# Kernel optimization log

Measured on AMD Instinct MI355X. Metric: run time of the kernel, lower is better.

Reference implementation:

```python
import jax, jax.numpy as jnp
import numpy as np

N = 100000   # nodes
E = 3200000  # edges
CIN = 6
H = 256
G = 16       # graphs in batch
EPS = 1e-5


def setup_inputs() -> dict:
    key = jax.random.key(0)
    ks = jax.random.split(key, 16)
    inp = {
        'pos': jax.random.normal(ks[0], (N, 3), dtype=jnp.float32),
        'norm': jax.random.normal(ks[1], (N, 3), dtype=jnp.float32),
        'edge_index': jax.random.randint(ks[2], (2, E), 0, N, dtype=jnp.int64),
        'batch': jnp.sort(jax.random.randint(ks[3], (N,), 0, G, dtype=jnp.int64)),
        'bn0_g': jnp.ones((CIN,), jnp.float32), 'bn0_b': jnp.zeros((CIN,), jnp.float32),
    }
    dims = [(CIN, H), (H, H), (H, H), (H, H)]
    for i, (ci, co) in enumerate(dims, start=1):
        inp[f'W{i}'] = jax.random.normal(ks[3 + i], (ci, co), jnp.float32) * 0.05
        inp[f'b{i}'] = jnp.zeros((co,), jnp.float32)
        inp[f'bn{i}_g'] = jnp.ones((co,), jnp.float32)
        inp[f'bn{i}_b'] = jnp.zeros((co,), jnp.float32)
    return inp


def _bn(x, g, b):
    # BatchNorm1d, training mode: biased batch stats over node dim
    m = jnp.mean(x, axis=0)
    v = jnp.var(x, axis=0)
    return (x - m) * jax.lax.rsqrt(v + EPS) * g + b


def _gcn(x, W, bias, row, col, en, sl):
    # GCNConv: linear -> symmetric-normalized aggregation (with self loops) -> +bias
    xw = x @ W                                             # [N, C_out]
    agg = jax.ops.segment_sum(en[:, None] * xw[row], col, num_segments=N)
    return agg + sl[:, None] * xw + bias


def reference(pos, norm, edge_index, batch,
              bn0_g, bn0_b,
              W1, b1, bn1_g, bn1_b,
              W2, b2, bn2_g, bn2_b,
              W3, b3, bn3_g, bn3_b,
              W4, b4, bn4_g, bn4_b):
    row, col = edge_index[0], edge_index[1]
    # gcn_norm with self loops: deg includes +1 self loop weight
    deg = jax.ops.segment_sum(jnp.ones((E,), jnp.float32), col, num_segments=N) + 1.0
    dinv = jax.lax.rsqrt(deg)
    en = dinv[row] * dinv[col]   # edge norm
    sl = dinv * dinv             # self-loop norm

    x = jnp.concatenate([pos, norm], axis=1)   # [N, 6]
    x = _bn(x, bn0_g, bn0_b)
    for (W, b, g, be) in [(W1, b1, bn1_g, bn1_b), (W2, b2, bn2_g, bn2_b),
                          (W3, b3, bn3_g, bn3_b), (W4, b4, bn4_g, bn4_b)]:
        x = _bn(jax.nn.relu(_gcn(x, W, b, row, col, en, sl)), g, be)

    # global mean pool over graph ids
    sums = jax.ops.segment_sum(x, batch, num_segments=G)
    cnt = jax.ops.segment_sum(jnp.ones((N,), jnp.float32), batch, num_segments=G)
    return sums / jnp.maximum(cnt, 1.0)[:, None]
```

## Files before the change

### kernel.cpp

```cpp
#include <hip/hip_runtime.h>
#include <hip/hip_bf16.h>
#include <cstdint>

#define N_NODES 100000
#define NPAD    100032
#define N_EDGES 3200000
#define HID 256
#define NG 16
#define BN_EPS 1e-5f
#define B0 120
#define NB 391
#define SLABS 128
#define FPART 25000
#define LDSROW 264
#define AGB 2048
#define NGRP (N_NODES / 4)

typedef unsigned short u16;
using bf16x8 = __attribute__((ext_vector_type(8))) short;
using f32x4  = __attribute__((ext_vector_type(4))) float;

__device__ __forceinline__ float bf2f(u16 b) {
    return __uint_as_float(((unsigned)b) << 16);
}
__device__ __forceinline__ u16 f2bf(float f) {
    unsigned u = __float_as_uint(f);
    unsigned r = (u + 0x7FFFu + ((u >> 16) & 1u)) >> 16;
    return (u16)r;
}
__device__ __forceinline__ float4 ld_bf16x4(const u16* p) {
    ushort4 u = *reinterpret_cast<const ushort4*>(p);
    float4 f;
    f.x = bf2f(u.x); f.y = bf2f(u.y); f.z = bf2f(u.z); f.w = bf2f(u.w);
    return f;
}

__global__ void k_count(const int* __restrict__ coli, int* __restrict__ cnt) {
    int i = blockIdx.x * blockDim.x + threadIdx.x;
    int st = gridDim.x * blockDim.x;
    for (; i < N_EDGES; i += st) atomicAdd(&cnt[coli[i]], 1);
}

__global__ __launch_bounds__(256) void k_scanA(const int* __restrict__ cnt,
                                               int* __restrict__ bsum) {
    const int t = threadIdx.x;
    const int i = blockIdx.x * 256 + t;
    int v = (i < N_NODES) ? cnt[i] : 0;
    for (int o = 32; o > 0; o >>= 1) v += __shfl_down(v, o);
    __shared__ int ws[4];
    if ((t & 63) == 0) ws[t >> 6] = v;
    __syncthreads();
    if (t == 0) bsum[blockIdx.x] = ws[0] + ws[1] + ws[2] + ws[3];
}

__global__ __launch_bounds__(512) void k_scanB(const int* __restrict__ bsum,
                                               int* __restrict__ boff,
                                               int* __restrict__ ptrN) {
    const int t = threadIdx.x;
    const int ln = t & 63, wv = t >> 6;
    int v = (t < NB) ? bsum[t] : 0;
    int sc = v;
    for (int o = 1; o < 64; o <<= 1) { int u = __shfl_up(sc, o); if (ln >= o) sc += u; }
    __shared__ int ws[8], wx[9];
    if (ln == 63) ws[wv] = sc;
    __syncthreads();
    if (t == 0) { int a = 0; for (int k = 0; k < 8; ++k) { wx[k] = a; a += ws[k]; } wx[8] = a; }
    __syncthreads();
    int excl = wx[wv] + sc - v;
    if (t < NB) boff[t] = excl;
    if (t == 0) ptrN[0] = wx[8];
}

__global__ __launch_bounds__(256) void k_scanC(const int* __restrict__ cnt,
                                               const int* __restrict__ boff,
                                               int* __restrict__ ptr,
                                               int* __restrict__ ptr2,
                                               float* __restrict__ dinv) {
    const int t = threadIdx.x;
    const int i = blockIdx.x * 256 + t;
    const int ln = t & 63, wv = t >> 6;
    int v = (i < N_NODES) ? cnt[i] : 0;
    if (i < N_NODES) dinv[i] = rsqrtf((float)v + 1.0f);
    int sc = v;
    for (int o = 1; o < 64; o <<= 1) { int u = __shfl_up(sc, o); if (ln >= o) sc += u; }
    __shared__ int ws[4], wx[4];
    if (ln == 63) ws[wv] = sc;
    __syncthreads();
    if (t == 0) { int a = 0; for (int k = 0; k < 4; ++k) { wx[k] = a; a += ws[k]; } }
    __syncthreads();
    int excl = boff[blockIdx.x] + wx[wv] + sc - v;
    if (i < N_NODES) { ptr[i] = excl; ptr2[i] = excl; }
}

__global__ void k_fillp(const int* __restrict__ rowi, const int* __restrict__ coli,
                        int* __restrict__ ptr2, int* __restrict__ esrc, int lo) {
    int i = blockIdx.x * blockDim.x + threadIdx.x;
    int st = gridDim.x * blockDim.x;
    const int hi = lo + FPART;
    for (; i < N_EDGES; i += st) {
        int c = coli[i];
        if (c >= lo && c < hi) {
            int r = rowi[i];
            int p = atomicAdd(&ptr2[c], 1);
            esrc[p] = r;
        }
    }
}

__global__ __launch_bounds__(256) void k_bn0stats(const float* __restrict__ pos,
                                                  const float* __restrict__ nrm,
                                                  const int* __restrict__ batch,
                                                  float* __restrict__ part ,
                                                  int* __restrict__ cg) {
    __shared__ int h[NG];
    if (threadIdx.x < NG) h[threadIdx.x] = 0;
    __syncthreads();
    float s[6] = {0, 0, 0, 0, 0, 0}, q[6] = {0, 0, 0, 0, 0, 0};
    int i = blockIdx.x * blockDim.x + threadIdx.x;
    int stp = gridDim.x * blockDim.x;
    for (; i < N_NODES; i += stp) {
        float v;
        v = pos[i * 3 + 0]; s[0] += v; q[0] += v * v;
        v = pos[i * 3 + 1]; s[1] += v; q[1] += v * v;
        v = pos[i * 3 + 2]; s[2] += v; q[2] += v * v;
        v = nrm[i * 3 + 0]; s[3] += v; q[3] += v * v;
        v = nrm[i * 3 + 1]; s[4] += v; q[4] += v * v;
        v = nrm[i * 3 + 2]; s[5] += v; q[5] += v * v;
        atomicAdd(&h[batch[i]], 1);
    }
#pragma unroll
    for (int k = 0; k < 6; ++k) {
        for (int o = 32; o > 0; o >>= 1) { s[k] += __shfl_down(s[k], o); q[k] += __shfl_down(q[k], o); }
    }
    __shared__ float ls[4][12];
    const int wv = threadIdx.x >> 6;
    const int ln = threadIdx.x & 63;
    if (ln == 0) {
#pragma unroll
        for (int k = 0; k < 6; ++k) { ls[wv][k] = s[k]; ls[wv][6 + k] = q[k]; }
    }
    __syncthreads();
    if (threadIdx.x < 12)
        part[blockIdx.x * 12 + threadIdx.x] =
            ls[0][threadIdx.x] + ls[1][threadIdx.x] + ls[2][threadIdx.x] + ls[3][threadIdx.x];
    if (threadIdx.x < NG) {
        int v = h[threadIdx.x];
        if (v) atomicAdd(&cg[threadIdx.x], v);
    }
}

__global__ void k_fold6(const float* __restrict__ W,
                        const float* __restrict__ part, float invcnt,
                        const float* __restrict__ gamma, const float* __restrict__ beta,
                        float* __restrict__ Wf, float* __restrict__ rvB) {
    __shared__ float st[12];
    int c = threadIdx.x;
    if (c < 12) {
        float a = 0.f;
        for (int b = 0; b < B0; ++b) a += part[b * 12 + c];
        st[c] = a;
    }
    __syncthreads();
    float acc = 0.f;
    for (int k = 0; k < 6; ++k) {
        float m = st[k] * invcnt;
        float var = st[6 + k] * invcnt - m * m;
        float A = gamma[k] * rsqrtf(var + BN_EPS);
        float B = beta[k] - m * A;
        float w = W[k * HID + c];
        Wf[k * HID + c] = A * w;
        acc = fmaf(B, w, acc);
    }
    rvB[c] = acc;
}

__global__ void k_fold256(const float* __restrict__ W,
                          const float* __restrict__ partL , float invcnt,
                          const float* __restrict__ gamma, const float* __restrict__ beta,
                          u16* __restrict__ WhiT, u16* __restrict__ WloT,
                          float* __restrict__ rv) {
    __shared__ float ss[HID], sq[HID];
    int c = threadIdx.x;
    {
        float a = 0.f, b = 0.f;
#pragma unroll 4
        for (int bb = 0; bb < SLABS; ++bb) {
            a += partL[bb * 512 + c];
            b += partL[bb * 512 + HID + c];
        }
        ss[c] = a; sq[c] = b;
    }
    __syncthreads();
    float acc = 0.f;
    for (int k = 0; k < HID; ++k) {
        float m = ss[k] * invcnt;
        float var = sq[k] * invcnt - m * m;
        float A = gamma[k] * rsqrtf(var + BN_EPS);
        float B = beta[k] - m * A;
        float w = W[k * HID + c];
        float wf = A * w;
        u16 hi = f2bf(wf);
        WhiT[c * HID + k] = hi;
        WloT[c * HID + k] = f2bf(wf - bf2f(hi));
        acc = fmaf(B, w, acc);
    }
    rv[c] = acc;
}

__global__ __launch_bounds__(256) void k_l1fused(
    const float* __restrict__ pos, const float* __restrict__ nrm,
    const int* __restrict__ ptr, const int* __restrict__ esrc,
    const float* __restrict__ dinv, const float* __restrict__ Wf,
    const float* __restrict__ rvB, const float* __restrict__ b1,
    u16* __restrict__ out, float* __restrict__ partL) {
    const int wv = threadIdx.x >> 6;
    const int ln = threadIdx.x & 63;
    float w[6][4], rv4[4], bb4[4];
#pragma unroll
    for (int k = 0; k < 6; ++k) {
        float4 t = *reinterpret_cast<const float4*>(&Wf[k * HID + ln * 4]);
        w[k][0] = t.x; w[k][1] = t.y; w[k][2] = t.z; w[k][3] = t.w;
    }
    {
        float4 t = *reinterpret_cast<const float4*>(&rvB[ln * 4]);
        rv4[0] = t.x; rv4[1] = t.y; rv4[2] = t.z; rv4[3] = t.w;
        float4 u = *reinterpret_cast<const float4*>(&b1[ln * 4]);
        bb4[0] = u.x; bb4[1] = u.y; bb4[2] = u.z; bb4[3] = u.w;
    }
    float ssr[4] = {0, 0, 0, 0}, qqr[4] = {0, 0, 0, 0};
    for (int n = blockIdx.x * 4 + wv; n < N_NODES; n += AGB * 4) {
        const float dn = dinv[n];
        float z0 = 0, z1 = 0, z2 = 0, z3 = 0, z4 = 0, z5 = 0, t = 0;
        const int s_ = ptr[n], e_ = ptr[n + 1];
        for (int e = s_ + ln; e < e_; e += 64) {
            int src = esrc[e];
            float we = dn * dinv[src];
            z0 = fmaf(we, pos[src * 3 + 0], z0);
            z1 = fmaf(we, pos[src * 3 + 1], z1);
            z2 = fmaf(we, pos[src * 3 + 2], z2);
            z3 = fmaf(we, nrm[src * 3 + 0], z3);
            z4 = fmaf(we, nrm[src * 3 + 1], z4);
            z5 = fmaf(we, nrm[src * 3 + 2], z5);
            t += we;
        }
        if (ln == 0) {
            float sl = dn * dn;
            z0 = fmaf(sl, pos[n * 3 + 0], z0);
            z1 = fmaf(sl, pos[n * 3 + 1], z1);
            z2 = fmaf(sl, pos[n * 3 + 2], z2);
            z3 = fmaf(sl, nrm[n * 3 + 0], z3);
            z4 = fmaf(sl, nrm[n * 3 + 1], z4);
            z5 = fmaf(sl, nrm[n * 3 + 2], z5);
            t += sl;
        }
#pragma unroll
        for (int o = 1; o < 64; o <<= 1) {
            z0 += __shfl_xor(z0, o); z1 += __shfl_xor(z1, o); z2 += __shfl_xor(z2, o);
            z3 += __shfl_xor(z3, o); z4 += __shfl_xor(z4, o); z5 += __shfl_xor(z5, o);
            t  += __shfl_xor(t, o);
        }
        ushort4 o4;
#pragma unroll
        for (int j = 0; j < 4; ++j) {
            float oj = fmaf(t, rv4[j], bb4[j]);
            oj = fmaf(z0, w[0][j], oj); oj = fmaf(z1, w[1][j], oj); oj = fmaf(z2, w[2][j], oj);
            oj = fmaf(z3, w[3][j], oj); oj = fmaf(z4, w[4][j], oj); oj = fmaf(z5, w[5][j], oj);
            oj = fmaxf(oj, 0.f);
            ssr[j] += oj; qqr[j] = fmaf(oj, oj, qqr[j]);
            ((u16*)&o4)[j] = f2bf(oj);
        }
        *reinterpret_cast<ushort4*>(&out[(size_t)n * HID + ln * 4]) = o4;
    }
    __shared__ float sh[4 * 512];
    float* shw = &sh[wv * 512];
#pragma unroll
    for (int j = 0; j < 4; ++j) { shw[ln * 4 + j] = ssr[j]; shw[256 + ln * 4 + j] = qqr[j]; }
    __syncthreads();
    const int t = threadIdx.x;
    float S = sh[t] + sh[512 + t] + sh[1024 + t] + sh[1536 + t];
    float Q = sh[256 + t] + sh[768 + t] + sh[1280 + t] + sh[1792 + t];
    float* slab = &partL[(size_t)(blockIdx.x & (SLABS - 1)) * 512];
    atomicAdd(&slab[t], S);
    atomicAdd(&slab[256 + t], Q);
}

__global__ __launch_bounds__(256) void k_gemm_lds(
    const u16* __restrict__ X, const u16* __restrict__ WhiT,
    const u16* __restrict__ WloT, const float* __restrict__ rv,
    u16* __restrict__ out) {
    __shared__ u16 As[64 * LDSROW];
    const int tid = threadIdx.x;
    const int wv = tid >> 6;
    const int ln = tid & 63;
    const int row0 = blockIdx.x * 64;
    const int lr = ln & 15;
    const int lk = (ln >> 4) * 8;
    const int wcol0 = wv * 64;

#pragma unroll
    for (int i = 0; i < 8; ++i) {
        int chunk = i * 256 + tid;
        int r = chunk >> 5;
        int kc = chunk & 31;
        bf16x8 v = *reinterpret_cast<const bf16x8*>(&X[(size_t)(row0 + r) * HID + kc * 8]);
        *reinterpret_cast<bf16x8*>(&As[r * LDSROW + kc * 8]) = v;
    }
    __syncthreads();

    f32x4 acc[4][4] = {};
    for (int kk = 0; kk < HID; kk += 32) {
        bf16x8 a[4], bh[4], bl[4];
#pragma unroll
        for (int i = 0; i < 4; ++i)
            a[i] = *reinterpret_cast<const bf16x8*>(&As[(i * 16 + lr) * LDSROW + kk + lk]);
#pragma unroll
        for (int c = 0; c < 4; ++c) {
            int col = wcol0 + c * 16 + lr;
            bh[c] = *reinterpret_cast<const bf16x8*>(&WhiT[(size_t)col * HID + kk + lk]);
            bl[c] = *reinterpret_cast<const bf16x8*>(&WloT[(size_t)col * HID + kk + lk]);
        }
#pragma unroll
        for (int i = 0; i < 4; ++i)
#pragma unroll
            for (int c = 0; c < 4; ++c) {
                acc[i][c] = __builtin_amdgcn_mfma_f32_16x16x32_bf16(a[i], bh[c], acc[i][c], 0, 0, 0);
                acc[i][c] = __builtin_amdgcn_mfma_f32_16x16x32_bf16(a[i], bl[c], acc[i][c], 0, 0, 0);
            }
    }
    const int crow = (ln >> 4) * 4;
#pragma unroll
    for (int c = 0; c < 4; ++c) {
        int col = wcol0 + c * 16 + lr;
        float rvc = rv[col];
#pragma unroll
        for (int i = 0; i < 4; ++i) {
#pragma unroll
            for (int rg = 0; rg < 4; ++rg) {
                int r = row0 + i * 16 + crow + rg;
                out[(size_t)r * HID + col] = f2bf(acc[i][c][rg] + rvc);
            }
        }
    }
}

__global__ __launch_bounds__(256) void k_agg(
    const u16* __restrict__ xw, const int* __restrict__ ptr,
    const int* __restrict__ esrc, const float* __restrict__ dinv,
    const float* __restrict__ bias, u16* __restrict__ y,
    float* __restrict__ partL) {
    const int wv = threadIdx.x >> 6;
    const int ln = threadIdx.x & 63;
    float4 b = *reinterpret_cast<const float4*>(&bias[ln * 4]);
    float ssr[4] = {0, 0, 0, 0}, qqr[4] = {0, 0, 0, 0};
    for (int g = blockIdx.x; g < NGRP; g += AGB) {
        const int n = g * 4 + wv;
        const float dn = dinv[n];
        const size_t base = (size_t)n * HID + ln * 4;
        float4 v = ld_bf16x4(&xw[base]);
        const float sl = dn * dn;
        float a0 = v.x * sl, a1 = v.y * sl, a2 = v.z * sl, a3 = v.w * sl;
        const int s = ptr[n], e = ptr[n + 1];
        for (int bs = s; bs < e; bs += 64) {
            const int cnt = (e - bs < 64) ? e - bs : 64;
            int myidx = 0;
            float myw = 0.f;
            if (ln < cnt) {
                myidx = esrc[bs + ln];
                myw = dinv[myidx] * dn;
            }
            int j = 0;
            for (; j + 3 < cnt; j += 4) {
                int   s0 = __shfl(myidx, j),     s1 = __shfl(myidx, j + 1);
                int   s2 = __shfl(myidx, j + 2), s3 = __shfl(myidx, j + 3);
                float w0 = __shfl(myw, j),       w1 = __shfl(myw, j + 1);
                float w2 = __shfl(myw, j + 2),   w3 = __shfl(myw, j + 3);
                float4 u0 = ld_bf16x4(&xw[(size_t)s0 * HID + ln * 4]);
                float4 u1 = ld_bf16x4(&xw[(size_t)s1 * HID + ln * 4]);
                float4 u2 = ld_bf16x4(&xw[(size_t)s2 * HID + ln * 4]);
                float4 u3 = ld_bf16x4(&xw[(size_t)s3 * HID + ln * 4]);
                a0 = fmaf(w0, u0.x, a0); a1 = fmaf(w0, u0.y, a1);
                a2 = fmaf(w0, u0.z, a2); a3 = fmaf(w0, u0.w, a3);
                a0 = fmaf(w1, u1.x, a0); a1 = fmaf(w1, u1.y, a1);
                a2 = fmaf(w1, u1.z, a2); a3 = fmaf(w1, u1.w, a3);
                a0 = fmaf(w2, u2.x, a0); a1 = fmaf(w2, u2.y, a1);
                a2 = fmaf(w2, u2.z, a2); a3 = fmaf(w2, u2.w, a3);
                a0 = fmaf(w3, u3.x, a0); a1 = fmaf(w3, u3.y, a1);
                a2 = fmaf(w3, u3.z, a2); a3 = fmaf(w3, u3.w, a3);
            }
            for (; j < cnt; ++j) {
                int   s0 = __shfl(myidx, j);
                float w0 = __shfl(myw, j);
                float4 u0 = ld_bf16x4(&xw[(size_t)s0 * HID + ln * 4]);
                a0 = fmaf(w0, u0.x, a0); a1 = fmaf(w0, u0.y, a1);
                a2 = fmaf(w0, u0.z, a2); a3 = fmaf(w0, u0.w, a3);
            }
        }
        a0 = fmaxf(a0 + b.x, 0.f);
        a1 = fmaxf(a1 + b.y, 0.f);
        a2 = fmaxf(a2 + b.z, 0.f);
        a3 = fmaxf(a3 + b.w, 0.f);
        ssr[0] += a0; qqr[0] = fmaf(a0, a0, qqr[0]);
        ssr[1] += a1; qqr[1] = fmaf(a1, a1, qqr[1]);
        ssr[2] += a2; qqr[2] = fmaf(a2, a2, qqr[2]);
        ssr[3] += a3; qqr[3] = fmaf(a3, a3, qqr[3]);
        ushort4 o;
        o.x = f2bf(a0); o.y = f2bf(a1); o.z = f2bf(a2); o.w = f2bf(a3);
        *reinterpret_cast<ushort4*>(&y[base]) = o;
    }
    __shared__ float sh[4 * 512];
    float* shw = &sh[wv * 512];
#pragma unroll
    for (int j = 0; j < 4; ++j) { shw[ln * 4 + j] = ssr[j]; shw[256 + ln * 4 + j] = qqr[j]; }
    __syncthreads();
    const int t = threadIdx.x;
    float S = sh[t] + sh[512 + t] + sh[1024 + t] + sh[1536 + t];
    float Q = sh[256 + t] + sh[768 + t] + sh[1280 + t] + sh[1792 + t];
    float* slab = &partL[(size_t)(blockIdx.x & (SLABS - 1)) * 512];
    atomicAdd(&slab[t], S);
    atomicAdd(&slab[256 + t], Q);
}

__global__ __launch_bounds__(256) void k_pool(const u16* __restrict__ y,
                                              const int* __restrict__ batch,
                                              float* __restrict__ ps) {
    const int c = threadIdx.x;
    const int n0 = blockIdx.x * 98;
    if (n0 >= N_NODES) return;
    const int n1 = (n0 + 98 < N_NODES) ? n0 + 98 : N_NODES;
    int cur = batch[n0];
    float acc = 0.f;
    for (int n = n0; n < n1; ++n) {
        float v = bf2f(y[(size_t)n * HID + c]);
        int g = batch[n];
        if (g != cur) {
            atomicAdd(&ps[cur * HID + c], acc);
            acc = 0.f;
            cur = g;
        }
        acc += v;
    }
    atomicAdd(&ps[cur * HID + c], acc);
}

__global__ void k_final(const float* __restrict__ ps, const int* __restrict__ cg,
                        const float* __restrict__ partL, const float* __restrict__ gamma,
                        const float* __restrict__ beta, float* __restrict__ out) {
    __shared__ float ss[HID], sq[HID];
    const int c = threadIdx.x;
    {
        float a = 0.f, b = 0.f;
#pragma unroll 4
        for (int bb = 0; bb < SLABS; ++bb) {
            a += partL[bb * 512 + c];
            b += partL[bb * 512 + HID + c];
        }
        ss[c] = a; sq[c] = b;
    }
    __syncthreads();
    const float invn = 1.0f / (float)N_NODES;
    float m = ss[c] * invn;
    float var = sq[c] * invn - m * m;
    float A = gamma[c] * rsqrtf(var + BN_EPS);
    float B = beta[c] - m * A;
    for (int g = 0; g < NG; ++g) {
        float cn = (float)cg[g];
        float val = (A * ps[g * HID + c] + cn * B) / fmaxf(cn, 1.0f);
        out[g * HID + c] = val;
    }
}

extern "C" void kernel_launch(void* const* d_in, const int* in_sizes, int n_in,
                              void* d_out, int out_size, void* d_ws, size_t ws_size,
                              hipStream_t stream) {
    const float* pos   = (const float*)d_in[0];
    const float* nrm   = (const float*)d_in[1];
    const int*   ei    = (const int*)d_in[2];
    const int*   batch = (const int*)d_in[3];
    const float* bn0g  = (const float*)d_in[4];
    const float* bn0b  = (const float*)d_in[5];
    const float* W[4]   = {(const float*)d_in[6],  (const float*)d_in[10], (const float*)d_in[14], (const float*)d_in[18]};
    const float* bb[4]  = {(const float*)d_in[7],  (const float*)d_in[11], (const float*)d_in[15], (const float*)d_in[19]};
    const float* bg[4]  = {(const float*)d_in[8],  (const float*)d_in[12], (const float*)d_in[16], (const float*)d_in[20]};
    const float* bbt[4] = {(const float*)d_in[9],  (const float*)d_in[13], (const float*)d_in[17], (const float*)d_in[21]};

    char* wp = (char*)d_ws;
    auto alloc = [&](size_t bytes) {
        char* p = wp;
        wp += (bytes + 255) & ~(size_t)255;
        return p;
    };
    float* dinv  = (float*)alloc((size_t)N_NODES * 4);
    int*   cnt   = (int*)  alloc((size_t)N_NODES * 4);
    int*   ptr   = (int*)  alloc((size_t)(N_NODES + 1) * 4);
    int*   ptr2  = (int*)  alloc((size_t)N_NODES * 4);
    int*   esrc  = (int*)  alloc((size_t)N_EDGES * 4);
    int*   bsum  = (int*)  alloc((size_t)NB * 4);
    int*   boff  = (int*)  alloc((size_t)NB * 4);
    u16*   bufA  = (u16*)  alloc((size_t)NPAD * HID * 2);
    u16*   bufB  = (u16*)  alloc((size_t)NPAD * HID * 2);
    float* part0 = (float*)alloc((size_t)B0 * 12 * 4);
    float* partL = (float*)alloc((size_t)SLABS * 512 * 4);
    float* Wf1   = (float*)alloc((size_t)6 * HID * 4);
    u16*   WhiT  = (u16*)  alloc((size_t)HID * HID * 2);
    u16*   WloT  = (u16*)  alloc((size_t)HID * HID * 2);
    float* rv    = (float*)alloc(HID * 4);
    float* psz   = (float*)alloc((size_t)(NG * HID + NG) * 4);
    float* ps    = psz;
    int*   cg    = (int*)(psz + NG * HID);
    (void)ws_size; (void)in_sizes; (void)n_in; (void)out_size;

    const int* rowi = ei;
    const int* coli = ei + N_EDGES;

    hipMemsetAsync(cnt, 0, (size_t)N_NODES * 4, stream);
    hipMemsetAsync(psz, 0, (size_t)(NG * HID + NG) * 4, stream);
    hipMemsetAsync(partL, 0, (size_t)SLABS * 512 * 4, stream);

    k_count<<<2048, 256, 0, stream>>>(coli, cnt);
    k_scanA<<<NB, 256, 0, stream>>>(cnt, bsum);
    k_scanB<<<1, 512, 0, stream>>>(bsum, boff, &ptr[N_NODES]);
    k_scanC<<<NB, 256, 0, stream>>>(cnt, boff, ptr, ptr2, dinv);
    for (int p = 0; p < 4; ++p)
        k_fillp<<<1024, 256, 0, stream>>>(rowi, coli, ptr2, esrc, p * FPART);

    k_bn0stats<<<B0, 256, 0, stream>>>(pos, nrm, batch, part0, cg);
    k_fold6<<<1, 256, 0, stream>>>(W[0], part0, 1.0f / (float)N_NODES, bn0g, bn0b, Wf1, rv);
    k_l1fused<<<AGB, 256, 0, stream>>>(pos, nrm, ptr, esrc, dinv, Wf1, rv, bb[0], bufA, partL);

    for (int l = 0; l < 3; ++l) {
        k_fold256<<<1, 256, 0, stream>>>(W[l + 1], partL, 1.0f / (float)N_NODES,
                                         bg[l], bbt[l], WhiT, WloT, rv);
        hipMemsetAsync(partL, 0, (size_t)SLABS * 512 * 4, stream);
        k_gemm_lds<<<NPAD / 64, 256, 0, stream>>>(bufA, WhiT, WloT, rv, bufB);
        k_agg<<<AGB, 256, 0, stream>>>(bufB, ptr, esrc, dinv, bb[l + 1], bufA, partL);
    }

    k_pool<<<(N_NODES + 97) / 98, 256, 0, stream>>>(bufA, batch, ps);
    k_final<<<1, 256, 0, stream>>>(ps, cg, partL, bg[3], bbt[3], (float*)d_out);
}
```

Before: 1.580 ms.

## Add atomic work-stealing in aggregation kernels, parallelize weight fold, unroll gather by 8

The aggregation kernels now take node groups dynamically from a global atomic cursor instead of a fixed grid-stride loop. This targets load imbalance caused by uneven node degrees, at the cost of one atomic and two block barriers per group. The weight-fold kernel is split across 16 blocks so the transposed bf16 hi/lo weights are written in parallel, while block 0 still computes the bias vector serially. The k_agg gather loop is unrolled from 4 to 8 edges, so more independent row loads are in flight at some register cost.

```diff
diff --git a/kernel.cpp b/kernel.cpp
--- a/kernel.cpp
+++ b/kernel.cpp
@@ -15,6 +15,7 @@
 #define LDSROW 264
 #define AGB 2048
 #define NGRP (N_NODES / 4)
+#define FB 16
 
 typedef unsigned short u16;
 using bf16x8 = __attribute__((ext_vector_type(8))) short;
@@ -191,20 +192,30 @@
         ss[c] = a; sq[c] = b;
     }
     __syncthreads();
-    float acc = 0.f;
-    for (int k = 0; k < HID; ++k) {
+    const int k0 = blockIdx.x * (HID / FB);
+#pragma unroll
+    for (int kk = 0; kk < HID / FB; ++kk) {
+        int k = k0 + kk;
         float m = ss[k] * invcnt;
         float var = sq[k] * invcnt - m * m;
         float A = gamma[k] * rsqrtf(var + BN_EPS);
-        float B = beta[k] - m * A;
         float w = W[k * HID + c];
         float wf = A * w;
         u16 hi = f2bf(wf);
         WhiT[c * HID + k] = hi;
         WloT[c * HID + k] = f2bf(wf - bf2f(hi));
-        acc = fmaf(B, w, acc);
-    }
-    rv[c] = acc;
+    }
+    if (blockIdx.x == 0) {
+        float acc = 0.f;
+        for (int k = 0; k < HID; ++k) {
+            float m = ss[k] * invcnt;
+            float var = sq[k] * invcnt - m * m;
+            float A = gamma[k] * rsqrtf(var + BN_EPS);
+            float B = beta[k] - m * A;
+            acc = fmaf(B, W[k * HID + c], acc);
+        }
+        rv[c] = acc;
+    }
 }
 
 __global__ __launch_bounds__(256) void k_l1fused(
@@ -212,7 +223,7 @@
     const int* __restrict__ ptr, const int* __restrict__ esrc,
     const float* __restrict__ dinv, const float* __restrict__ Wf,
     const float* __restrict__ rvB, const float* __restrict__ b1,
-    u16* __restrict__ out, float* __restrict__ partL) {
+    u16* __restrict__ out, float* __restrict__ partL, int* __restrict__ cursor) {
     const int wv = threadIdx.x >> 6;
     const int ln = threadIdx.x & 63;
     float w[6][4], rv4[4], bb4[4];
@@ -228,7 +239,14 @@
         bb4[0] = u.x; bb4[1] = u.y; bb4[2] = u.z; bb4[3] = u.w;
     }
     float ssr[4] = {0, 0, 0, 0}, qqr[4] = {0, 0, 0, 0};
-    for (int n = blockIdx.x * 4 + wv; n < N_NODES; n += AGB * 4) {
+    __shared__ int sg;
+    for (;;) {
+        if (threadIdx.x == 0) sg = atomicAdd(cursor, 1);
+        __syncthreads();
+        const int g = sg;
+        __syncthreads();
+        if (g >= NGRP) break;
+        const int n = g * 4 + wv;
         const float dn = dinv[n];
         float z0 = 0, z1 = 0, z2 = 0, z3 = 0, z4 = 0, z5 = 0, t = 0;
         const int s_ = ptr[n], e_ = ptr[n + 1];
@@ -347,12 +365,18 @@
     const u16* __restrict__ xw, const int* __restrict__ ptr,
     const int* __restrict__ esrc, const float* __restrict__ dinv,
     const float* __restrict__ bias, u16* __restrict__ y,
-    float* __restrict__ partL) {
+    float* __restrict__ partL, int* __restrict__ cursor) {
     const int wv = threadIdx.x >> 6;
     const int ln = threadIdx.x & 63;
     float4 b = *reinterpret_cast<const float4*>(&bias[ln * 4]);
     float ssr[4] = {0, 0, 0, 0}, qqr[4] = {0, 0, 0, 0};
-    for (int g = blockIdx.x; g < NGRP; g += AGB) {
+    __shared__ int sg;
+    for (;;) {
+        if (threadIdx.x == 0) sg = atomicAdd(cursor, 1);
+        __syncthreads();
+        const int g = sg;
+        __syncthreads();
+        if (g >= NGRP) break;
         const int n = g * 4 + wv;
         const float dn = dinv[n];
         const size_t base = (size_t)n * HID + ln * 4;
@@ -369,15 +393,23 @@
                 myw = dinv[myidx] * dn;
             }
             int j = 0;
-            for (; j + 3 < cnt; j += 4) {
+            for (; j + 7 < cnt; j += 8) {
                 int   s0 = __shfl(myidx, j),     s1 = __shfl(myidx, j + 1);
                 int   s2 = __shfl(myidx, j + 2), s3 = __shfl(myidx, j + 3);
+                int   s4 = __shfl(myidx, j + 4), s5 = __shfl(myidx, j + 5);
+                int   s6 = __shfl(myidx, j + 6), s7 = __shfl(myidx, j + 7);
                 float w0 = __shfl(myw, j),       w1 = __shfl(myw, j + 1);
                 float w2 = __shfl(myw, j + 2),   w3 = __shfl(myw, j + 3);
+                float w4 = __shfl(myw, j + 4),   w5 = __shfl(myw, j + 5);
+                float w6 = __shfl(myw, j + 6),   w7 = __shfl(myw, j + 7);
                 float4 u0 = ld_bf16x4(&xw[(size_t)s0 * HID + ln * 4]);
                 float4 u1 = ld_bf16x4(&xw[(size_t)s1 * HID + ln * 4]);
                 float4 u2 = ld_bf16x4(&xw[(size_t)s2 * HID + ln * 4]);
                 float4 u3 = ld_bf16x4(&xw[(size_t)s3 * HID + ln * 4]);
+                float4 u4 = ld_bf16x4(&xw[(size_t)s4 * HID + ln * 4]);
+                float4 u5 = ld_bf16x4(&xw[(size_t)s5 * HID + ln * 4]);
+                float4 u6 = ld_bf16x4(&xw[(size_t)s6 * HID + ln * 4]);
+                float4 u7 = ld_bf16x4(&xw[(size_t)s7 * HID + ln * 4]);
                 a0 = fmaf(w0, u0.x, a0); a1 = fmaf(w0, u0.y, a1);
                 a2 = fmaf(w0, u0.z, a2); a3 = fmaf(w0, u0.w, a3);
                 a0 = fmaf(w1, u1.x, a0); a1 = fmaf(w1, u1.y, a1);
@@ -386,6 +418,14 @@
                 a2 = fmaf(w2, u2.z, a2); a3 = fmaf(w2, u2.w, a3);
                 a0 = fmaf(w3, u3.x, a0); a1 = fmaf(w3, u3.y, a1);
                 a2 = fmaf(w3, u3.z, a2); a3 = fmaf(w3, u3.w, a3);
+                a0 = fmaf(w4, u4.x, a0); a1 = fmaf(w4, u4.y, a1);
+                a2 = fmaf(w4, u4.z, a2); a3 = fmaf(w4, u4.w, a3);
+                a0 = fmaf(w5, u5.x, a0); a1 = fmaf(w5, u5.y, a1);
+                a2 = fmaf(w5, u5.z, a2); a3 = fmaf(w5, u5.w, a3);
+                a0 = fmaf(w6, u6.x, a0); a1 = fmaf(w6, u6.y, a1);
+                a2 = fmaf(w6, u6.z, a2); a3 = fmaf(w6, u6.w, a3);
+                a0 = fmaf(w7, u7.x, a0); a1 = fmaf(w7, u7.y, a1);
+                a2 = fmaf(w7, u7.z, a2); a3 = fmaf(w7, u7.w, a3);
             }
             for (; j < cnt; ++j) {
                 int   s0 = __shfl(myidx, j);
@@ -504,16 +544,17 @@
     u16*   WhiT  = (u16*)  alloc((size_t)HID * HID * 2);
     u16*   WloT  = (u16*)  alloc((size_t)HID * HID * 2);
     float* rv    = (float*)alloc(HID * 4);
-    float* psz   = (float*)alloc((size_t)(NG * HID + NG) * 4);
+    float* psz   = (float*)alloc((size_t)(NG * HID + NG + 8) * 4);
     float* ps    = psz;
     int*   cg    = (int*)(psz + NG * HID);
+    int*   curs  = (int*)(psz + NG * HID + NG);
     (void)ws_size; (void)in_sizes; (void)n_in; (void)out_size;
 
     const int* rowi = ei;
     const int* coli = ei + N_EDGES;
 
     hipMemsetAsync(cnt, 0, (size_t)N_NODES * 4, stream);
-    hipMemsetAsync(psz, 0, (size_t)(NG * HID + NG) * 4, stream);
+    hipMemsetAsync(psz, 0, (size_t)(NG * HID + NG + 8) * 4, stream);
     hipMemsetAsync(partL, 0, (size_t)SLABS * 512 * 4, stream);
 
     k_count<<<2048, 256, 0, stream>>>(coli, cnt);
@@ -525,14 +566,16 @@
 
     k_bn0stats<<<B0, 256, 0, stream>>>(pos, nrm, batch, part0, cg);
     k_fold6<<<1, 256, 0, stream>>>(W[0], part0, 1.0f / (float)N_NODES, bn0g, bn0b, Wf1, rv);
-    k_l1fused<<<AGB, 256, 0, stream>>>(pos, nrm, ptr, esrc, dinv, Wf1, rv, bb[0], bufA, partL);
+    k_l1fused<<<AGB, 256, 0, stream>>>(pos, nrm, ptr, esrc, dinv, Wf1, rv, bb[0], bufA,
+                                       partL, &curs[0]);
 
     for (int l = 0; l < 3; ++l) {
-        k_fold256<<<1, 256, 0, stream>>>(W[l + 1], partL, 1.0f / (float)N_NODES,
-                                         bg[l], bbt[l], WhiT, WloT, rv);
+        k_fold256<<<FB, 256, 0, stream>>>(W[l + 1], partL, 1.0f / (float)N_NODES,
+                                          bg[l], bbt[l], WhiT, WloT, rv);
         hipMemsetAsync(partL, 0, (size_t)SLABS * 512 * 4, stream);
         k_gemm_lds<<<NPAD / 64, 256, 0, stream>>>(bufA, WhiT, WloT, rv, bufB);
-        k_agg<<<AGB, 256, 0, stream>>>(bufB, ptr, esrc, dinv, bb[l + 1], bufA, partL);
+        k_agg<<<AGB, 256, 0, stream>>>(bufB, ptr, esrc, dinv, bb[l + 1], bufA,
+                                       partL, &curs[1 + l]);
     }
 
     k_pool<<<(N_NODES + 97) / 98, 256, 0, stream>>>(bufA, batch, ps);
```

Measured after the change: 2.073 ms. 31.3% more time.
